# Kernel optimization log

Measured on AMD Instinct MI355X. Metric: run time of the kernel, lower is better.

The kernel has to match this reference:

```python
import jax, jax.numpy as jnp
import numpy as np

D_MODEL = 1024
NUM_HEADS = 16
HEAD_DIM = D_MODEL // NUM_HEADS


def setup_inputs() -> dict:
    key = jax.random.key(0)
    ks = jax.random.split(key, 9)
    B, S = 4, 2048
    s = 1.0 / np.sqrt(D_MODEL)
    return {
        "x": jax.random.normal(ks[0], (B, S, D_MODEL), dtype=jnp.float32),
        "Wq": jax.random.normal(ks[1], (D_MODEL, D_MODEL), dtype=jnp.float32) * s,
        "bq": jnp.zeros((D_MODEL,), dtype=jnp.float32),
        "Wk": jax.random.normal(ks[2], (D_MODEL, D_MODEL), dtype=jnp.float32) * s,
        "bk": jnp.zeros((D_MODEL,), dtype=jnp.float32),
        "Wv": jax.random.normal(ks[3], (D_MODEL, D_MODEL), dtype=jnp.float32) * s,
        "bv": jnp.zeros((D_MODEL,), dtype=jnp.float32),
        "Wo": jax.random.normal(ks[4], (D_MODEL, D_MODEL), dtype=jnp.float32) * s,
        "bo": jnp.zeros((D_MODEL,), dtype=jnp.float32),
    }


def reference(x, Wq, bq, Wk, bk, Wv, bv, Wo, bo):
    B, S, D = x.shape
    H, Hd = NUM_HEADS, HEAD_DIM
    # projections: [B,S,D] -> [B,H,S,Hd]
    def split_heads(t):
        return t.reshape(B, S, H, Hd).transpose(0, 2, 1, 3)
    q = split_heads(x @ Wq + bq)
    k = split_heads(x @ Wk + bk)
    v = split_heads(x @ Wv + bv)
    scale = 1.0 / jnp.sqrt(jnp.asarray(Hd, dtype=x.dtype))
    scores = jnp.einsum("bhsd,bhtd->bhst", q, k) * scale  # [B,H,S,S]
    attn = jax.nn.softmax(scores, axis=-1)
    ctx = jnp.einsum("bhst,bhtd->bhsd", attn, v)  # [B,H,S,Hd]
    ctx = ctx.transpose(0, 2, 1, 3).reshape(B, S, D)
    return ctx @ Wo + bo
```

## Files before the change

kernel.cpp:

```cpp
#include <hip/hip_runtime.h>
#include <hip/hip_bf16.h>
#include <stdint.h>


typedef __bf16 bf16;
typedef __bf16 bf16x8 __attribute__((ext_vector_type(8)));
typedef float  f32x4  __attribute__((ext_vector_type(4)));
typedef float  f32x16 __attribute__((ext_vector_type(16)));

#define XB_OFF   (0ull)
#define WT_OFF   (16ull << 20)
#define Q_OFF    (24ull << 20)
#define K_OFF    (40ull << 20)
#define V_OFF    (56ull << 20)
#define CTX_OFF  (72ull << 20)

#define QSCALE 0.18033688011112042591f

__device__ __forceinline__ void gload_lds16(const void* g, void* l) {
  __builtin_amdgcn_global_load_lds(
      (const __attribute__((address_space(1))) void*)g,
      (__attribute__((address_space(3))) void*)l, 16, 0, 0);
}

__global__ __launch_bounds__(256) void cvt_x(const float* __restrict__ x,
                                             bf16* __restrict__ xb) {
  int i = blockIdx.x * 256 + threadIdx.x;
  const float4* p = (const float4*)x;
  float4 a = p[(size_t)i * 2];
  float4 b = p[(size_t)i * 2 + 1];
  bf16x8 o;
  o[0] = (bf16)a.x; o[1] = (bf16)a.y; o[2] = (bf16)a.z; o[3] = (bf16)a.w;
  o[4] = (bf16)b.x; o[5] = (bf16)b.y; o[6] = (bf16)b.z; o[7] = (bf16)b.w;
  *((bf16x8*)xb + i) = o;
}

__global__ __launch_bounds__(256) void cvt_w(const float* __restrict__ w0,
                                             const float* __restrict__ w1,
                                             const float* __restrict__ w2,
                                             const float* __restrict__ w3,
                                             bf16* __restrict__ wt) {
  int z = blockIdx.z;
  const float* W = (z == 0) ? w0 : (z == 1) ? w1 : (z == 2) ? w2 : w3;
  bf16* Wt = wt + (size_t)z * 1024 * 1024;
  __shared__ float tile[64][65];
  int i0 = blockIdx.y * 64, o0 = blockIdx.x * 64;
  int tid = threadIdx.x;
#pragma unroll
  for (int rep = 0; rep < 16; rep++) {
    int idx = rep * 256 + tid;
    int r = idx >> 6, c = idx & 63;
    tile[r][c] = W[(size_t)(i0 + r) * 1024 + o0 + c];
  }
  __syncthreads();
#pragma unroll
  for (int rep = 0; rep < 16; rep++) {
    int idx = rep * 256 + tid;
    int r = idx >> 6, c = idx & 63;
    Wt[(size_t)(o0 + r) * 1024 + i0 + c] = (bf16)tile[c][r];
  }
}

template <int MODE>
__global__ __launch_bounds__(256, 2) void gemm_bt(
    const bf16* __restrict__ A, const bf16* __restrict__ Bt,
    const float* __restrict__ b0, const float* __restrict__ b1,
    const float* __restrict__ b2,
    bf16* __restrict__ Qo, bf16* __restrict__ Ko, bf16* __restrict__ Vo,
    float* __restrict__ out) {
  __shared__ __align__(16) bf16 a_lds[128 * 64];
  __shared__ __align__(16) bf16 b_lds[128 * 64];
  int tid = threadIdx.x;
  int lane = tid & 63, wid = tid >> 6;
  int wr = wid >> 1, wc = wid & 1;
  int g = lane >> 4, rlo = lane & 15;
  int m0 = blockIdx.x * 128, n0 = blockIdx.y * 128;

  f32x4 acc[4][4] = {};
  const char* Ab = (const char*)A;
  const char* Bb = (const char*)Bt;

  for (int k0 = 0; k0 < 1024; k0 += 64) {
#pragma unroll
    for (int rep = 0; rep < 4; rep++) {
      int idx = rep * 256 + tid;
      int row = idx >> 3;
      int sw = ((idx & 7) * 16) ^ ((row & 7) << 4);
      gload_lds16(Ab + ((size_t)(m0 + row) * 1024 + k0) * 2 + sw,
                  (char*)a_lds + (size_t)idx * 16);
    }
#pragma unroll
    for (int rep = 0; rep < 4; rep++) {
      int idx = rep * 256 + tid;
      int row = idx >> 3;
      int sw = ((idx & 7) * 16) ^ ((row & 7) << 4);
      gload_lds16(Bb + ((size_t)(n0 + row) * 1024 + k0) * 2 + sw,
                  (char*)b_lds + (size_t)idx * 16);
    }
    __syncthreads();
#pragma unroll
    for (int ks = 0; ks < 2; ks++) {
      bf16x8 af[4], bfr[4];
#pragma unroll
      for (int mt = 0; mt < 4; mt++) {
        int row = wr * 64 + mt * 16 + rlo;
        int koff = (ks * 32 + g * 8) ^ ((row & 7) << 3);
        af[mt] = *(const bf16x8*)&a_lds[row * 64 + koff];
      }
#pragma unroll
      for (int nt = 0; nt < 4; nt++) {
        int row = wc * 64 + nt * 16 + rlo;
        int koff = (ks * 32 + g * 8) ^ ((row & 7) << 3);
        bfr[nt] = *(const bf16x8*)&b_lds[row * 64 + koff];
      }
#pragma unroll
      for (int mt = 0; mt < 4; mt++)
#pragma unroll
        for (int nt = 0; nt < 4; nt++)
          acc[mt][nt] = __builtin_amdgcn_mfma_f32_16x16x32_bf16(
              af[mt], bfr[nt], acc[mt][nt], 0, 0, 0);
    }
    __syncthreads();
  }

#pragma unroll
  for (int nt = 0; nt < 4; nt++) {
    int n = n0 + wc * 64 + nt * 16 + rlo;
    if (MODE == 0) {
      int which = n >> 10, nn = n & 1023;
      const float* bp = (which == 0) ? b0 : (which == 1) ? b1 : b2;
      float bias = bp[nn];
      bf16* dst = (which == 0) ? Qo : (which == 1) ? Ko : Vo;
      float scale = (which == 0) ? QSCALE : 1.0f;
      int h = nn >> 6, hd = nn & 63;
#pragma unroll
      for (int mt = 0; mt < 4; mt++) {
#pragma unroll
        for (int r = 0; r < 4; r++) {
          int m = m0 + wr * 64 + mt * 16 + g * 4 + r;
          int bb = m >> 11, ss = m & 2047;
          float v = (acc[mt][nt][r] + bias) * scale;
          dst[(((size_t)(bb * 16 + h) * 2048 + ss) << 6) + hd] = (bf16)v;
        }
      }
    } else {
      float bias = b0[n];
#pragma unroll
      for (int mt = 0; mt < 4; mt++) {
#pragma unroll
        for (int r = 0; r < 4; r++) {
          int m = m0 + wr * 64 + mt * 16 + g * 4 + r;
          out[(size_t)m * 1024 + n] = acc[mt][nt][r] + bias;
        }
      }
    }
  }
}

__global__ __launch_bounds__(256) void vtr2(const bf16* __restrict__ V,
                                            bf16* __restrict__ V2) {
  __shared__ bf16 t[64][72];
  int bh = blockIdx.y, s0 = blockIdx.x * 64;
  int tid = threadIdx.x;
  const bf16* Vb = V + ((size_t)bh * 2048 + s0) * 64;
#pragma unroll
  for (int rep = 0; rep < 2; rep++) {
    int idx = rep * 256 + tid;
    int s = idx >> 3, dv = (idx & 7) * 8;
    bf16x8 v = *(const bf16x8*)&Vb[(size_t)s * 64 + dv];
#pragma unroll
    for (int j = 0; j < 8; j++) t[s][dv + j] = v[j];
  }
  __syncthreads();
  int f = tid >> 6, l = tid & 63;
  int dh = f >> 1, ks = f & 1;
  int chunk = (2 * ks + (l >> 5)) & 3;
  int d = dh * 32 + (l & 31);
#pragma unroll
  for (int tt = 0; tt < 2; tt++) {
    bf16x8 v;
#pragma unroll
    for (int e = 0; e < 8; e++) {
      int sl = chunk * 8 + e;
      int sp = (sl & ~12) | ((sl & 4) << 1) | ((sl & 8) >> 1);
      v[e] = t[tt * 32 + sp][d];
    }
    size_t T = (size_t)(s0 >> 5) + tt;
    *(bf16x8*)&V2[(((size_t)bh * 64 + T) * 4 + f) * 512 + l * 8] = v;
  }
}

__global__ __launch_bounds__(256, 4) void attn(const bf16* __restrict__ Q,
                                               const bf16* __restrict__ K,
                                               const bf16* __restrict__ V2,
                                               bf16* __restrict__ ctx) {
  __shared__ __align__(16) bf16 kbuf[2][32 * 64];
  int tid = threadIdx.x;
  int lane = tid & 63, wid = tid >> 6;
  int r31 = lane & 31, half = lane >> 5;
  int wg = blockIdx.x;
  int virt = (wg & 7) * 128 + (wg >> 3);
  int bh = virt >> 4, qt = virt & 15;
  int qbase = qt * 128 + wid * 32;

  const char* Kg = (const char*)(K + (size_t)bh * 2048 * 64);
  const bf16* V2b = V2 + (size_t)bh * 64 * 4 * 512;

  int krow = tid >> 3;
  size_t kofs = (size_t)krow * 128 + (((tid & 7) ^ (krow & 7)) << 4);

  int kread[4];
#pragma unroll
  for (int ks = 0; ks < 4; ks++)
    kread[ks] = r31 * 64 + (((2 * ks + half) ^ (r31 & 7)) << 3);

  const bf16* qrow = Q + ((size_t)bh * 2048 + qbase + r31) * 64 + half * 8;
  bf16x8 qa[4];
#pragma unroll
  for (int ks = 0; ks < 4; ks++) qa[ks] = *(const bf16x8*)&qrow[ks * 16];

  f32x16 o0 = {}, o1 = {};
  f32x4 lvec = {};

#define KSTAGE(BUF, T0)                                                       \
  gload_lds16(Kg + (size_t)(T0) * 128 + kofs, (char*)kbuf[BUF] + tid * 16)

  KSTAGE(0, 0);
  bf16x8 vf[4];
#pragma unroll
  for (int f = 0; f < 4; f++)
    vf[f] = *(const bf16x8*)&V2b[(size_t)f * 512 + lane * 8];
  __syncthreads();

  int cur = 0;
  for (int it = 0; it < 64; ++it) {
    int t1 = (it + 1) & 63;
    KSTAGE(cur ^ 1, t1 * 32);
    bf16x8 vn[4];
#pragma unroll
    for (int f = 0; f < 4; f++)
      vn[f] = *(const bf16x8*)&V2b[((size_t)t1 * 4 + f) * 512 + lane * 8];

    const bf16* kb = kbuf[cur];
    f32x16 s = {};
    __builtin_amdgcn_s_setprio(1);
#pragma unroll
    for (int ks = 0; ks < 4; ks++) {
      bf16x8 kf = *(const bf16x8*)&kb[kread[ks]];
      s = __builtin_amdgcn_mfma_f32_32x32x16_bf16(kf, qa[ks], s, 0, 0, 0);
    }
    __builtin_amdgcn_s_setprio(0);

#pragma unroll
    for (int i = 0; i < 16; i++) s[i] = __builtin_amdgcn_exp2f(s[i]);
#pragma unroll
    for (int i = 0; i < 4; i++)
      lvec[i] += (s[i] + s[i + 4]) + (s[i + 8] + s[i + 12]);

    bf16x8 pa0, pa1;
#pragma unroll
    for (int i = 0; i < 8; i++) {
      pa0[i] = (bf16)s[i];
      pa1[i] = (bf16)s[8 + i];
    }

    __builtin_amdgcn_s_setprio(1);
    o0 = __builtin_amdgcn_mfma_f32_32x32x16_bf16(pa0, vf[0], o0, 0, 0, 0);
    o0 = __builtin_amdgcn_mfma_f32_32x32x16_bf16(pa1, vf[1], o0, 0, 0, 0);
    o1 = __builtin_amdgcn_mfma_f32_32x32x16_bf16(pa0, vf[2], o1, 0, 0, 0);
    o1 = __builtin_amdgcn_mfma_f32_32x32x16_bf16(pa1, vf[3], o1, 0, 0, 0);
    __builtin_amdgcn_s_setprio(0);

    __syncthreads();
#pragma unroll
    for (int f = 0; f < 4; f++) vf[f] = vn[f];
    cur ^= 1;
  }
#undef KSTAGE

  float l = (lvec[0] + lvec[1]) + (lvec[2] + lvec[3]);
  l += __shfl_xor(l, 32);
  float inv = 1.0f / l;
  int b = bh >> 4, h = bh & 15;
#pragma unroll
  for (int r = 0; r < 16; r++) {
    int ql = (r & 3) + 8 * (r >> 2) + 4 * half;
    float iv = __shfl(inv, ql);
    size_t base = (((size_t)(b * 2048 + qbase + ql)) << 10) + h * 64 + r31;
    ctx[base] = (bf16)(o0[r] * iv);
    ctx[base + 32] = (bf16)(o1[r] * iv);
  }
}

extern "C" void kernel_launch(void* const* d_in, const int* in_sizes, int n_in,
                              void* d_out, int out_size, void* d_ws, size_t ws_size,
                              hipStream_t stream) {
  const float* x  = (const float*)d_in[0];
  const float* Wq = (const float*)d_in[1];
  const float* bq = (const float*)d_in[2];
  const float* Wk = (const float*)d_in[3];
  const float* bk = (const float*)d_in[4];
  const float* Wv = (const float*)d_in[5];
  const float* bv = (const float*)d_in[6];
  const float* Wo = (const float*)d_in[7];
  const float* bo = (const float*)d_in[8];
  float* out = (float*)d_out;
  char* ws = (char*)d_ws;

  bf16* xb  = (bf16*)(ws + XB_OFF);
  bf16* wt  = (bf16*)(ws + WT_OFF);
  bf16* Qb  = (bf16*)(ws + Q_OFF);
  bf16* Kb  = (bf16*)(ws + K_OFF);
  bf16* Vb  = (bf16*)(ws + V_OFF);
  bf16* cx  = (bf16*)(ws + CTX_OFF);
  bf16* V2b = (bf16*)(ws + XB_OFF);

  cvt_x<<<4096, 256, 0, stream>>>(x, xb);
  cvt_w<<<dim3(16, 16, 4), 256, 0, stream>>>(Wq, Wk, Wv, Wo, wt);
  gemm_bt<0><<<dim3(64, 24), 256, 0, stream>>>(xb, wt, bq, bk, bv,
                                               Qb, Kb, Vb, nullptr);
  vtr2<<<dim3(32, 64), 256, 0, stream>>>(Vb, V2b);
  attn<<<1024, 256, 0, stream>>>(Qb, Kb, V2b, cx);
  gemm_bt<1><<<dim3(64, 8), 256, 0, stream>>>(cx, wt + 3ull * 1024 * 1024, bo,
                                              nullptr, nullptr, nullptr,
                                              nullptr, nullptr, out);
}
```

Baseline: 176.1 us.

## Fuse V transpose into QKV GEMM epilogue and unroll attention loop by two

The QKV projection epilogue now writes V straight into the permuted MFMA-friendly layout the attention kernel consumes, so the separate vtr2 transpose kernel and its extra read/write pass over V are gone. The attention main loop is also manually unrolled by two with fixed double-buffer indices and named V register sets, replacing the runtime buffer toggle and the register copy of the prefetched V fragments. The scattered V stores in the GEMM epilogue may coalesce worse than before.

Result: slower. 308.0 us (+74.9%).

```diff
diff --git a/kernel.cpp b/kernel.cpp
--- a/kernel.cpp
+++ b/kernel.cpp
@@ -130,7 +130,6 @@
       int which = n >> 10, nn = n & 1023;
       const float* bp = (which == 0) ? b0 : (which == 1) ? b1 : b2;
       float bias = bp[nn];
-      bf16* dst = (which == 0) ? Qo : (which == 1) ? Ko : Vo;
       float scale = (which == 0) ? QSCALE : 1.0f;
       int h = nn >> 6, hd = nn & 63;
 #pragma unroll
@@ -140,7 +139,19 @@
           int m = m0 + wr * 64 + mt * 16 + g * 4 + r;
           int bb = m >> 11, ss = m & 2047;
           float v = (acc[mt][nt][r] + bias) * scale;
-          dst[(((size_t)(bb * 16 + h) * 2048 + ss) << 6) + hd] = (bf16)v;
+          int bh64 = bb * 16 + h;
+          if (which == 2) {
+            int T = ss >> 5;
+            int x = ss & 31;
+            int sl = (x & ~12) | ((x & 4) << 1) | ((x & 8) >> 1);
+            int chunk = sl >> 3, e = sl & 7;
+            int l = ((chunk & 1) << 5) + (hd & 31);
+            int f = ((hd >> 5) << 1) + (chunk >> 1);
+            Vo[(((size_t)bh64 * 64 + T) * 4 + f) * 512 + l * 8 + e] = (bf16)v;
+          } else {
+            bf16* dst = (which == 0) ? Qo : Ko;
+            dst[(((size_t)bh64 * 2048 + ss) << 6) + hd] = (bf16)v;
+          }
         }
       }
     } else {
@@ -154,39 +165,6 @@
         }
       }
     }
-  }
-}
-
-__global__ __launch_bounds__(256) void vtr2(const bf16* __restrict__ V,
-                                            bf16* __restrict__ V2) {
-  __shared__ bf16 t[64][72];
-  int bh = blockIdx.y, s0 = blockIdx.x * 64;
-  int tid = threadIdx.x;
-  const bf16* Vb = V + ((size_t)bh * 2048 + s0) * 64;
-#pragma unroll
-  for (int rep = 0; rep < 2; rep++) {
-    int idx = rep * 256 + tid;
-    int s = idx >> 3, dv = (idx & 7) * 8;
-    bf16x8 v = *(const bf16x8*)&Vb[(size_t)s * 64 + dv];
-#pragma unroll
-    for (int j = 0; j < 8; j++) t[s][dv + j] = v[j];
-  }
-  __syncthreads();
-  int f = tid >> 6, l = tid & 63;
-  int dh = f >> 1, ks = f & 1;
-  int chunk = (2 * ks + (l >> 5)) & 3;
-  int d = dh * 32 + (l & 31);
-#pragma unroll
-  for (int tt = 0; tt < 2; tt++) {
-    bf16x8 v;
-#pragma unroll
-    for (int e = 0; e < 8; e++) {
-      int sl = chunk * 8 + e;
-      int sp = (sl & ~12) | ((sl & 4) << 1) | ((sl & 8) >> 1);
-      v[e] = t[tt * 32 + sp][d];
-    }
-    size_t T = (size_t)(s0 >> 5) + tt;
-    *(bf16x8*)&V2[(((size_t)bh * 64 + T) * 4 + f) * 512 + l * 8] = v;
   }
 }
 
@@ -225,58 +203,61 @@
 #define KSTAGE(BUF, T0)                                                       \
   gload_lds16(Kg + (size_t)(T0) * 128 + kofs, (char*)kbuf[BUF] + tid * 16)
 
+#define VLOAD(VF, T0)                                                         \
+  do {                                                                        \
+    VF##0 = *(const bf16x8*)&V2b[((size_t)(T0) * 4 + 0) * 512 + lane * 8];    \
+    VF##1 = *(const bf16x8*)&V2b[((size_t)(T0) * 4 + 1) * 512 + lane * 8];    \
+    VF##2 = *(const bf16x8*)&V2b[((size_t)(T0) * 4 + 2) * 512 + lane * 8];    \
+    VF##3 = *(const bf16x8*)&V2b[((size_t)(T0) * 4 + 3) * 512 + lane * 8];    \
+  } while (0)
+
+#define COMPUTE(KB, V0, V1, V2_, V3)                                          \
+  do {                                                                        \
+    const bf16* kb = KB;                                                      \
+    f32x16 s = {};                                                            \
+    __builtin_amdgcn_s_setprio(1);                                            \
+    _Pragma("unroll") for (int ks = 0; ks < 4; ks++) {                        \
+      bf16x8 kf = *(const bf16x8*)&kb[kread[ks]];                             \
+      s = __builtin_amdgcn_mfma_f32_32x32x16_bf16(kf, qa[ks], s, 0, 0, 0);    \
+    }                                                                         \
+    __builtin_amdgcn_s_setprio(0);                                            \
+    _Pragma("unroll") for (int i = 0; i < 16; i++)                            \
+        s[i] = __builtin_amdgcn_exp2f(s[i]);                                  \
+    _Pragma("unroll") for (int i = 0; i < 4; i++)                             \
+        lvec[i] += (s[i] + s[i + 4]) + (s[i + 8] + s[i + 12]);                \
+    bf16x8 pa0, pa1;                                                          \
+    _Pragma("unroll") for (int i = 0; i < 8; i++) {                           \
+      pa0[i] = (bf16)s[i];                                                    \
+      pa1[i] = (bf16)s[8 + i];                                                \
+    }                                                                         \
+    __builtin_amdgcn_s_setprio(1);                                            \
+    o0 = __builtin_amdgcn_mfma_f32_32x32x16_bf16(pa0, V0, o0, 0, 0, 0);       \
+    o0 = __builtin_amdgcn_mfma_f32_32x32x16_bf16(pa1, V1, o0, 0, 0, 0);       \
+    o1 = __builtin_amdgcn_mfma_f32_32x32x16_bf16(pa0, V2_, o1, 0, 0, 0);      \
+    o1 = __builtin_amdgcn_mfma_f32_32x32x16_bf16(pa1, V3, o1, 0, 0, 0);       \
+    __builtin_amdgcn_s_setprio(0);                                            \
+  } while (0)
+
+  bf16x8 vfA0, vfA1, vfA2, vfA3, vfB0, vfB1, vfB2, vfB3;
+
   KSTAGE(0, 0);
-  bf16x8 vf[4];
-#pragma unroll
-  for (int f = 0; f < 4; f++)
-    vf[f] = *(const bf16x8*)&V2b[(size_t)f * 512 + lane * 8];
+  VLOAD(vfA, 0);
   __syncthreads();
 
-  int cur = 0;
-  for (int it = 0; it < 64; ++it) {
-    int t1 = (it + 1) & 63;
-    KSTAGE(cur ^ 1, t1 * 32);
-    bf16x8 vn[4];
-#pragma unroll
-    for (int f = 0; f < 4; f++)
-      vn[f] = *(const bf16x8*)&V2b[((size_t)t1 * 4 + f) * 512 + lane * 8];
-
-    const bf16* kb = kbuf[cur];
-    f32x16 s = {};
-    __builtin_amdgcn_s_setprio(1);
-#pragma unroll
-    for (int ks = 0; ks < 4; ks++) {
-      bf16x8 kf = *(const bf16x8*)&kb[kread[ks]];
-      s = __builtin_amdgcn_mfma_f32_32x32x16_bf16(kf, qa[ks], s, 0, 0, 0);
-    }
-    __builtin_amdgcn_s_setprio(0);
-
-#pragma unroll
-    for (int i = 0; i < 16; i++) s[i] = __builtin_amdgcn_exp2f(s[i]);
-#pragma unroll
-    for (int i = 0; i < 4; i++)
-      lvec[i] += (s[i] + s[i + 4]) + (s[i + 8] + s[i + 12]);
-
-    bf16x8 pa0, pa1;
-#pragma unroll
-    for (int i = 0; i < 8; i++) {
-      pa0[i] = (bf16)s[i];
-      pa1[i] = (bf16)s[8 + i];
-    }
-
-    __builtin_amdgcn_s_setprio(1);
-    o0 = __builtin_amdgcn_mfma_f32_32x32x16_bf16(pa0, vf[0], o0, 0, 0, 0);
-    o0 = __builtin_amdgcn_mfma_f32_32x32x16_bf16(pa1, vf[1], o0, 0, 0, 0);
-    o1 = __builtin_amdgcn_mfma_f32_32x32x16_bf16(pa0, vf[2], o1, 0, 0, 0);
-    o1 = __builtin_amdgcn_mfma_f32_32x32x16_bf16(pa1, vf[3], o1, 0, 0, 0);
-    __builtin_amdgcn_s_setprio(0);
-
+  for (int it = 0; it < 64; it += 2) {
+    KSTAGE(1, (it + 1) * 32);
+    VLOAD(vfB, it + 1);
+    COMPUTE(kbuf[0], vfA0, vfA1, vfA2, vfA3);
     __syncthreads();
-#pragma unroll
-    for (int f = 0; f < 4; f++) vf[f] = vn[f];
-    cur ^= 1;
+    int t2 = (it + 2) & 63;
+    KSTAGE(0, t2 * 32);
+    VLOAD(vfA, t2);
+    COMPUTE(kbuf[1], vfB0, vfB1, vfB2, vfB3);
+    __syncthreads();
   }
 #undef KSTAGE
+#undef VLOAD
+#undef COMPUTE
 
   float l = (lvec[0] + lvec[1]) + (lvec[2] + lvec[3]);
   l += __shfl_xor(l, 32);
@@ -311,15 +292,13 @@
   bf16* wt  = (bf16*)(ws + WT_OFF);
   bf16* Qb  = (bf16*)(ws + Q_OFF);
   bf16* Kb  = (bf16*)(ws + K_OFF);
-  bf16* Vb  = (bf16*)(ws + V_OFF);
+  bf16* V2b = (bf16*)(ws + V_OFF);
   bf16* cx  = (bf16*)(ws + CTX_OFF);
-  bf16* V2b = (bf16*)(ws + XB_OFF);
 
   cvt_x<<<4096, 256, 0, stream>>>(x, xb);
   cvt_w<<<dim3(16, 16, 4), 256, 0, stream>>>(Wq, Wk, Wv, Wo, wt);
   gemm_bt<0><<<dim3(64, 24), 256, 0, stream>>>(xb, wt, bq, bk, bv,
-                                               Qb, Kb, Vb, nullptr);
-  vtr2<<<dim3(32, 64), 256, 0, stream>>>(Vb, V2b);
+                                               Qb, Kb, V2b, nullptr);
   attn<<<1024, 256, 0, stream>>>(Qb, Kb, V2b, cx);
   gemm_bt<1><<<dim3(64, 8), 256, 0, stream>>>(cx, wt + 3ull * 1024 * 1024, bo,
                                               nullptr, nullptr, nullptr,
```
